# Kernel tuning notes

Hardware: AMD Instinct MI355X
Metric: run time of the kernel (lower is better)

The kernel has to match this reference:

```python
import jax, jax.numpy as jnp
import numpy as np

N, E, H, D_IN, D_OUT, DEPTH, G = 100000, 1600000, 128, 128, 10, 3, 256


def setup_inputs() -> dict:
    key = jax.random.key(0)
    ks = jax.random.split(key, 16)
    s = lambda k, shape: jax.random.normal(k, shape, dtype=jnp.float32) * 0.05
    inp = {
        "x": jax.random.normal(ks[0], (N, D_IN), dtype=jnp.float32),
        "edge_index": jax.random.randint(ks[1], (2, E), 0, N, dtype=jnp.int32),
        "control_edge_index": jax.random.randint(ks[2], (2, 1024), 0, N, dtype=jnp.int32),
        "batch": jnp.sort(jax.random.randint(ks[3], (N,), 0, G, dtype=jnp.int32)),
        # encoder MLP: input_dim -> hidden -> hidden
        "enc_w1": s(ks[4], (D_IN, H)), "enc_b1": jnp.zeros((H,), jnp.float32),
        "enc_w2": s(ks[5], (H, H)),    "enc_b2": jnp.zeros((H,), jnp.float32),
        # conv_depth GCN layers, hidden -> hidden
        "conv_w": s(ks[6], (DEPTH, H, H)), "conv_b": jnp.zeros((DEPTH, H), jnp.float32),
        # decoder MLP: hidden -> hidden -> output_dim
        "dec_w1": s(ks[7], (H, H)),     "dec_b1": jnp.zeros((H,), jnp.float32),
        "dec_w2": s(ks[8], (H, D_OUT)), "dec_b2": jnp.zeros((D_OUT,), jnp.float32),
    }
    return inp


def _gcn_forward(x, enc_w1, enc_b1, enc_w2, enc_b2, conv_w, conv_b,
                 dec_w1, dec_b1, dec_w2, dec_b2, edge_index, batch):
    # encoder MLP (Linear-ReLU-Dropout(eval)-Linear)
    h = jax.nn.relu(x @ enc_w1 + enc_b1) @ enc_w2 + enc_b2

    # GCN normalization with self-loops: D^{-1/2} (A + I) D^{-1/2}
    loops = jnp.arange(N, dtype=edge_index.dtype)
    src = jnp.concatenate([edge_index[0], loops])  # [E + N]
    dst = jnp.concatenate([edge_index[1], loops])
    deg = jax.ops.segment_sum(jnp.ones_like(src, dtype=h.dtype), dst, num_segments=N)
    inv_sqrt = jax.lax.rsqrt(deg)  # deg >= 1 thanks to self-loops
    coef = (inv_sqrt[src] * inv_sqrt[dst])[:, None]  # [E+N, 1]

    for l in range(DEPTH):
        hw = h @ conv_w[l] + conv_b[l]                      # [N, H]
        h = jax.ops.segment_sum(hw[src] * coef, dst, num_segments=N)
        if l < DEPTH - 1:  # linear=False -> nonlinearity between convs
            h = jax.nn.relu(h)

    # global_add_pool over graph ids
    pooled = jax.ops.segment_sum(h, batch, num_segments=G)   # [G, H]

    # decoder MLP
    return jax.nn.relu(pooled @ dec_w1 + dec_b1) @ dec_w2 + dec_b2  # [G, D_OUT]


def reference(x, edge_index, control_edge_index, batch, enc_w1, enc_b1, enc_w2,
              enc_b2, conv_w, conv_b, dec_w1, dec_b1, dec_w2, dec_b2):
    # control_edge_index corresponds to the (disabled) control mechanism; unused
    return _gcn_forward(x, enc_w1, enc_b1, enc_w2, enc_b2, conv_w, conv_b,
                        dec_w1, dec_b1, dec_w2, dec_b2, edge_index, batch)
```

## Files before the change

kernel.cpp:

```cpp
#include <hip/hip_runtime.h>
#include <hip/hip_bf16.h>
#include <cstdint>
#include <cstddef>

#define NN 100000
#define NE 1600000
#define HH 128
#define NG 256

#define NB 196
#define BSH 9
#define BMSK 511
#define CHUNK 16384
#define NBLK 98

typedef __bf16 bf16x8 __attribute__((ext_vector_type(8)));
typedef float floatx4 __attribute__((ext_vector_type(4)));

__device__ __forceinline__ uint32_t f2b(float f) {
  union { float f; uint32_t u; } v; v.f = f;
  uint32_t u = v.u;
  return (u + 0x7FFFu + ((u >> 16) & 1u)) >> 16;
}
__device__ __forceinline__ float b2f(uint32_t h) {
  union { uint32_t u; float f; } v; v.u = h << 16;
  return v.f;
}
__device__ __forceinline__ void addrow(float* a, uint4 v) {
  a[0] += b2f(v.x & 0xFFFFu); a[1] += b2f(v.x >> 16);
  a[2] += b2f(v.y & 0xFFFFu); a[3] += b2f(v.y >> 16);
  a[4] += b2f(v.z & 0xFFFFu); a[5] += b2f(v.z >> 16);
  a[6] += b2f(v.w & 0xFFFFu); a[7] += b2f(v.w >> 16);
}


__global__ __launch_bounds__(256) void k_cntA(const int* __restrict__ src,
                                              int* __restrict__ blkcnt) {
  __shared__ int h[NB];
  int t = threadIdx.x;
  if (t < NB) h[t] = 0;
  __syncthreads();
  int base = blockIdx.x * CHUNK, end = min(base + CHUNK, NE);
  for (int i = base + t; i < end; i += 256) atomicAdd(&h[src[i] >> BSH], 1);
  __syncthreads();
  if (t < NB) blkcnt[blockIdx.x * NB + t] = h[t];
}

__global__ __launch_bounds__(256) void k_cntB(const uint2* __restrict__ pairs,
                                              int* __restrict__ blkcnt) {
  __shared__ int h[NB];
  int t = threadIdx.x;
  if (t < NB) h[t] = 0;
  __syncthreads();
  int base = blockIdx.x * CHUNK, end = min(base + CHUNK, NE);
  for (int i = base + t; i < end; i += 256) atomicAdd(&h[pairs[i].y >> BSH], 1);
  __syncthreads();
  if (t < NB) blkcnt[blockIdx.x * NB + t] = h[t];
}

__global__ __launch_bounds__(64) void k_colscan(const int* __restrict__ blkcnt,
                                                int* __restrict__ poff,
                                                int* __restrict__ colsum) {
  int b = blockIdx.x, t = threadIdx.x;
  int carry = 0;
  for (int base = 0; base < NBLK; base += 64) {
    int r = base + t;
    int x = (r < NBLK) ? blkcnt[r * NB + b] : 0;
    int v = x;
    for (int d = 1; d < 64; d <<= 1) { int u = __shfl_up(v, d); if (t >= d) v += u; }
    if (r < NBLK) poff[r * NB + b] = carry + v - x;
    carry += __shfl(v, 63);
  }
  if (t == 0) colsum[b] = carry;
}

__global__ void k_gscan(const int* __restrict__ colsum, int* __restrict__ gbase,
                        int* __restrict__ off, int set_off) {
  __shared__ int s[256];
  int t = threadIdx.x;
  int x = (t < NB) ? colsum[t] : 0;
  s[t] = x; __syncthreads();
  for (int d = 1; d < 256; d <<= 1) {
    int v = (t >= d) ? s[t - d] : 0;
    __syncthreads();
    s[t] += v;
    __syncthreads();
  }
  if (t < NB) gbase[t] = s[t] - x;
  if (t == 0) { gbase[NB] = NE; if (set_off) off[NN] = NE; }
}

__global__ __launch_bounds__(256) void k_placeA(const int* __restrict__ src,
                                                const int* __restrict__ dst,
                                                const int* __restrict__ poff,
                                                const int* __restrict__ gbase,
                                                uint2* __restrict__ pairs) {
  __shared__ int cur[NB];
  int t = threadIdx.x;
  if (t < NB) cur[t] = poff[blockIdx.x * NB + t] + gbase[t];
  __syncthreads();
  int base = blockIdx.x * CHUNK, end = min(base + CHUNK, NE);
  for (int i = base + t; i < end; i += 256) {
    int s = src[i], d = dst[i];
    int p = atomicAdd(&cur[s >> BSH], 1);
    pairs[p] = make_uint2((unsigned)s, (unsigned)d);
  }
}

__global__ __launch_bounds__(256) void k_placeB(const uint2* __restrict__ pairs,
                                                const int* __restrict__ poff,
                                                const int* __restrict__ gbase,
                                                uint32_t* __restrict__ outb) {
  __shared__ int cur[NB];
  int t = threadIdx.x;
  if (t < NB) cur[t] = poff[blockIdx.x * NB + t] + gbase[t];
  __syncthreads();
  int base = blockIdx.x * CHUNK, end = min(base + CHUNK, NE);
  for (int i = base + t; i < end; i += 256) {
    uint2 v = pairs[i];
    int p = atomicAdd(&cur[v.y >> BSH], 1);
    outb[p] = v.x | ((v.y & (unsigned)BMSK) << 17);
  }
}

__global__ __launch_bounds__(256) void k_bucket_sort(
    const uint32_t* __restrict__ pairbuf, const int* __restrict__ gbase,
    const int* __restrict__ batch,
    int* __restrict__ off, float* __restrict__ inv, int* __restrict__ csrs,
    int* __restrict__ dhist2, int* __restrict__ gstart)
{
  __shared__ int cnt[512];
  __shared__ int loff[512];
  __shared__ int psum[256];
  int b = blockIdx.x;
  int tid = threadIdx.x;
  cnt[tid] = 0; cnt[tid + 256] = 0;
  __syncthreads();
  int s0 = gbase[b], s1 = gbase[b + 1];
  for (int i = s0 + tid; i < s1; i += 256)
    atomicAdd(&cnt[pairbuf[i] >> 17], 1);
  __syncthreads();
  int a0 = cnt[2 * tid], a1 = cnt[2 * tid + 1];
  int s = a0 + a1;
  psum[tid] = s;
  __syncthreads();
  for (int d = 1; d < 256; d <<= 1) {
    int v = (tid >= d) ? psum[tid - d] : 0;
    __syncthreads();
    psum[tid] += v;
    __syncthreads();
  }
  int excl = psum[tid] - s;
  loff[2 * tid] = excl;
  loff[2 * tid + 1] = excl + a0;
  __syncthreads();
  int* h64 = psum;
  if (tid < 64) h64[tid] = 0;
  __syncthreads();
#pragma unroll
  for (int k = 0; k < 2; ++k) {
    int i = tid + k * 256;
    int node = b * 512 + i;
    if (node < NN) {
      off[node] = s0 + loff[i];
      inv[node] = rsqrtf((float)cnt[i] + 1.0f);
      int d = cnt[i]; if (d > 63) d = 63;
      atomicAdd(&h64[d], 1);
    }
  }
  {
    int n0 = b * 512, n1 = min(n0 + 512, NN);
    for (int i = n0 + tid; i < n1; i += 256) {
      int bb = batch[i];
      if (i == 0) { for (int g = 0; g <= bb; ++g) gstart[g] = 0; }
      else { int aa = batch[i - 1]; for (int g = aa + 1; g <= bb; ++g) gstart[g] = i; }
      if (i == NN - 1) { for (int g = bb + 1; g <= NG; ++g) gstart[g] = NN; }
    }
  }
  __syncthreads();
  if (tid < 64) dhist2[b * 64 + tid] = h64[tid];
  cnt[tid] = loff[tid]; cnt[tid + 256] = loff[tid + 256];
  __syncthreads();
  for (int i = s0 + tid; i < s1; i += 256) {
    uint32_t v = pairbuf[i];
    int p = atomicAdd(&cnt[v >> 17], 1);
    csrs[s0 + p] = (int)(v & 0x1FFFFu);
  }
}

__global__ void k_dscan(const int* __restrict__ dhist2, int* __restrict__ dcur) {
  int t = threadIdx.x;
  int sum = 0;
  for (int r = 0; r < NB; ++r) sum += dhist2[r * 64 + (63 - t)];
  int v = sum;
  for (int d = 1; d < 64; d <<= 1) { int u = __shfl_up(v, d); if (t >= d) v += u; }
  dcur[63 - t] = v - sum;
}

__global__ __launch_bounds__(256) void k_dplace(const int* __restrict__ off,
                                                int* __restrict__ dcur,
                                                int* __restrict__ order) {
  __shared__ int h[64], base[64];
  int t = threadIdx.x;
  if (t < 64) h[t] = 0;
  __syncthreads();
  int i = blockIdx.x * 256 + t;
  int d = 0, ld = 0;
  if (i < NN) { d = off[i + 1] - off[i]; if (d > 63) d = 63; ld = atomicAdd(&h[d], 1); }
  __syncthreads();
  if (t < 64) base[t] = h[t] ? atomicAdd(&dcur[t], h[t]) : 0;
  __syncthreads();
  if (i < NN) order[base[d] + ld] = i;
}

__global__ __launch_bounds__(256) void k_gemm(
    const uint16_t* __restrict__ A16, const float* __restrict__ A32,
    const float* __restrict__ W, const float* __restrict__ bias,
    const float* __restrict__ scale,
    uint16_t* __restrict__ Out, int M, int do_relu)
{
  __shared__ uint16_t Wt[128][136];
  const int tid = threadIdx.x;

  for (int it = 0; it < 16; ++it) {
    int idx = tid + it * 256;
    int n = idx & 127;
    int k0 = (idx >> 7) * 4;
    uint2 wv;
    wv.x = f2b(W[(k0 + 0) * 128 + n]) | (f2b(W[(k0 + 1) * 128 + n]) << 16);
    wv.y = f2b(W[(k0 + 2) * 128 + n]) | (f2b(W[(k0 + 3) * 128 + n]) << 16);
    *(uint2*)&Wt[n][k0] = wv;
  }
  __syncthreads();

  const int lane = tid & 63;
  const int wave = tid >> 6;
  const int lrow = lane & 15;
  const int quad = lane >> 4;
  const int lk = quad * 8;
  const int row0 = blockIdx.x * 128 + wave * 32;

  floatx4 acc[2][8];
#pragma unroll
  for (int t = 0; t < 2; ++t)
#pragma unroll
    for (int n = 0; n < 8; ++n)
      acc[t][n] = (floatx4){0.f, 0.f, 0.f, 0.f};

#pragma unroll
  for (int ks = 0; ks < 4; ++ks) {
    bf16x8 a[2];
#pragma unroll
    for (int t = 0; t < 2; ++t) {
      int r = row0 + t * 16 + lrow;
      uint4 tmp = {0u, 0u, 0u, 0u};
      if (r < M) {
        if (A32) {
          float4 f0 = *(const float4*)(A32 + (size_t)r * HH + ks * 32 + lk);
          float4 f1 = *(const float4*)(A32 + (size_t)r * HH + ks * 32 + lk + 4);
          tmp.x = f2b(f0.x) | (f2b(f0.y) << 16);
          tmp.y = f2b(f0.z) | (f2b(f0.w) << 16);
          tmp.z = f2b(f1.x) | (f2b(f1.y) << 16);
          tmp.w = f2b(f1.z) | (f2b(f1.w) << 16);
        } else {
          tmp = *(const uint4*)(A16 + (size_t)r * HH + ks * 32 + lk);
        }
      }
      a[t] = __builtin_bit_cast(bf16x8, tmp);
    }
#pragma unroll
    for (int n = 0; n < 8; ++n) {
      bf16x8 b = __builtin_bit_cast(bf16x8, *(const uint4*)&Wt[n * 16 + lrow][ks * 32 + lk]);
      acc[0][n] = __builtin_amdgcn_mfma_f32_16x16x32_bf16(b, a[0], acc[0][n], 0, 0, 0);
      acc[1][n] = __builtin_amdgcn_mfma_f32_16x16x32_bf16(b, a[1], acc[1][n], 0, 0, 0);
    }
  }

  float4 b4[8];
#pragma unroll
  for (int n = 0; n < 8; ++n) b4[n] = *(const float4*)(bias + n * 16 + quad * 4);

#pragma unroll
  for (int t = 0; t < 2; ++t) {
    int row = row0 + t * 16 + lrow;
    if (row < M) {
      float sc = scale ? scale[row] : 1.0f;
      uint16_t* orow = Out + (size_t)row * HH;
#pragma unroll
      for (int n = 0; n < 8; ++n) {
        float v0 = acc[t][n][0] + b4[n].x;
        float v1 = acc[t][n][1] + b4[n].y;
        float v2 = acc[t][n][2] + b4[n].z;
        float v3 = acc[t][n][3] + b4[n].w;
        if (do_relu) {
          v0 = fmaxf(v0, 0.f); v1 = fmaxf(v1, 0.f);
          v2 = fmaxf(v2, 0.f); v3 = fmaxf(v3, 0.f);
        }
        v0 *= sc; v1 *= sc; v2 *= sc; v3 *= sc;
        uint2 o;
        o.x = f2b(v0) | (f2b(v1) << 16);
        o.y = f2b(v2) | (f2b(v3) << 16);
        *(uint2*)(orow + n * 16 + quad * 4) = o;
      }
    }
  }
}

__global__ __launch_bounds__(256) void k_agg(
    const uint16_t* __restrict__ hw2, const int* __restrict__ off,
    const int* __restrict__ csrs, const float* __restrict__ inv,
    const int* __restrict__ order,
    uint16_t* __restrict__ hout, int do_relu)
{
  int slot = blockIdx.x * 16 + (threadIdx.x >> 4);
  if (slot >= NN) return;
  int node = order[slot];
  int c = (threadIdx.x & 15) * 8;

  uint4 sv = *(const uint4*)(hw2 + (size_t)node * HH + c);
  float a[8] = {0.f, 0.f, 0.f, 0.f, 0.f, 0.f, 0.f, 0.f};
  addrow(a, sv);

  int e0 = off[node], e1 = off[node + 1];
  int e = e0;
  for (; e + 4 <= e1; e += 4) {
    int s0 = csrs[e + 0], s1 = csrs[e + 1], s2 = csrs[e + 2], s3 = csrs[e + 3];
    uint4 v0 = *(const uint4*)(hw2 + (size_t)s0 * HH + c);
    uint4 v1 = *(const uint4*)(hw2 + (size_t)s1 * HH + c);
    uint4 v2 = *(const uint4*)(hw2 + (size_t)s2 * HH + c);
    uint4 v3 = *(const uint4*)(hw2 + (size_t)s3 * HH + c);
    addrow(a, v0); addrow(a, v1); addrow(a, v2); addrow(a, v3);
  }
  for (; e < e1; ++e) {
    int s = csrs[e];
    uint4 v = *(const uint4*)(hw2 + (size_t)s * HH + c);
    addrow(a, v);
  }
  float invd = inv[node];
#pragma unroll
  for (int j = 0; j < 8; ++j) {
    a[j] *= invd;
    if (do_relu) a[j] = fmaxf(a[j], 0.f);
  }
  uint4 o;
  o.x = f2b(a[0]) | (f2b(a[1]) << 16);
  o.y = f2b(a[2]) | (f2b(a[3]) << 16);
  o.z = f2b(a[4]) | (f2b(a[5]) << 16);
  o.w = f2b(a[6]) | (f2b(a[7]) << 16);
  *(uint4*)(hout + (size_t)node * HH + c) = o;
}

__global__ __launch_bounds__(256) void k_pooldec(
    const uint16_t* __restrict__ h, const int* __restrict__ gstart,
    const float* __restrict__ w1, const float* __restrict__ b1,
    const float* __restrict__ w2, const float* __restrict__ b2,
    float* __restrict__ out)
{
  __shared__ float red[16][132];
  __shared__ float p[128], tmpv[128];
  int g = blockIdx.x;
  int tid = threadIdx.x;
  int slot = tid >> 4;
  int c = (tid & 15) * 8;

  int r0 = gstart[g], r1 = gstart[g + 1];
  float a[8] = {0.f, 0.f, 0.f, 0.f, 0.f, 0.f, 0.f, 0.f};
  for (int r = r0 + slot; r < r1; r += 16) {
    uint4 v = *(const uint4*)(h + (size_t)r * HH + c);
    a[0] += b2f(v.x & 0xFFFFu); a[1] += b2f(v.x >> 16);
    a[2] += b2f(v.y & 0xFFFFu); a[3] += b2f(v.y >> 16);
    a[4] += b2f(v.z & 0xFFFFu); a[5] += b2f(v.z >> 16);
    a[6] += b2f(v.w & 0xFFFFu); a[7] += b2f(v.w >> 16);
  }
  *(float4*)&red[slot][c]     = make_float4(a[0], a[1], a[2], a[3]);
  *(float4*)&red[slot][c + 4] = make_float4(a[4], a[5], a[6], a[7]);
  __syncthreads();
  if (tid < 128) {
    float s = 0.f;
#pragma unroll
    for (int k = 0; k < 16; ++k) s += red[k][tid];
    p[tid] = s;
  }
  __syncthreads();
  if (tid < 128) {
    float acc1 = b1[tid];
    for (int k = 0; k < 128; ++k) acc1 += p[k] * w1[k * 128 + tid];
    tmpv[tid] = fmaxf(acc1, 0.f);
  }
  __syncthreads();
  if (tid < 10) {
    float o = b2[tid];
    for (int k = 0; k < 128; ++k) o += tmpv[k] * w2[k * 10 + tid];
    out[g * 10 + tid] = o;
  }
}

extern "C" void kernel_launch(void* const* d_in, const int* in_sizes, int n_in,
                              void* d_out, int out_size, void* d_ws, size_t ws_size,
                              hipStream_t stream) {
  const float* x       = (const float*)d_in[0];
  const int*   eidx    = (const int*)d_in[1];
  const int*   src     = eidx;
  const int*   dst     = eidx + NE;
  const int*   batch   = (const int*)d_in[3];
  const float* enc_w1  = (const float*)d_in[4];
  const float* enc_b1  = (const float*)d_in[5];
  const float* enc_w2  = (const float*)d_in[6];
  const float* enc_b2  = (const float*)d_in[7];
  const float* conv_w  = (const float*)d_in[8];
  const float* conv_b  = (const float*)d_in[9];
  const float* dec_w1  = (const float*)d_in[10];
  const float* dec_b1  = (const float*)d_in[11];
  const float* dec_w2  = (const float*)d_in[12];
  const float* dec_b2  = (const float*)d_in[13];
  float* out = (float*)d_out;

  char* ws = (char*)d_ws;
  size_t o = 0;
  auto alloc = [&](size_t bytes) -> char* {
    char* p = ws + o;
    o += (bytes + 255) & ~(size_t)255;
    return p;
  };
  int*      off     = (int*)alloc((size_t)(NN + 1) * 4);
  int*      csrs    = (int*)alloc((size_t)NE * 4);
  float*    inv     = (float*)alloc((size_t)NN * 4);
  int*      blkcntA = (int*)alloc((size_t)NBLK * NB * 4);
  int*      poffA   = (int*)alloc((size_t)NBLK * NB * 4);
  int*      blkcntB = (int*)alloc((size_t)NBLK * NB * 4);
  int*      poffB   = (int*)alloc((size_t)NBLK * NB * 4);
  int*      colsumA = (int*)alloc((size_t)NB * 4);
  int*      colsumB = (int*)alloc((size_t)NB * 4);
  int*      gbaseA  = (int*)alloc((size_t)(NB + 1) * 4);
  int*      gbaseB  = (int*)alloc((size_t)(NB + 1) * 4);
  int*      dhist2  = (int*)alloc((size_t)NB * 64 * 4);
  int*      dcur    = (int*)alloc(64 * 4);
  int*      order   = (int*)alloc((size_t)NN * 4);
  int*      gstart  = (int*)alloc((size_t)(NG + 1) * 4);
  uint16_t* buf0    = (uint16_t*)alloc((size_t)NN * HH * 2);
  uint16_t* buf1    = (uint16_t*)alloc((size_t)NN * HH * 2);
  uint2*    pairsA  = (uint2*)buf1;
  uint32_t* pairB   = (uint32_t*)((char*)buf1 + (size_t)NE * 8);

  k_cntA<<<dim3(NBLK), dim3(256), 0, stream>>>(src, blkcntA);
  k_colscan<<<dim3(NB), dim3(64), 0, stream>>>(blkcntA, poffA, colsumA);
  k_gscan<<<dim3(1), dim3(256), 0, stream>>>(colsumA, gbaseA, off, 0);
  k_placeA<<<dim3(NBLK), dim3(256), 0, stream>>>(src, dst, poffA, gbaseA, pairsA);
  k_cntB<<<dim3(NBLK), dim3(256), 0, stream>>>(pairsA, blkcntB);
  k_colscan<<<dim3(NB), dim3(64), 0, stream>>>(blkcntB, poffB, colsumB);
  k_gscan<<<dim3(1), dim3(256), 0, stream>>>(colsumB, gbaseB, off, 1);
  k_placeB<<<dim3(NBLK), dim3(256), 0, stream>>>(pairsA, poffB, gbaseB, pairB);
  k_bucket_sort<<<dim3(NB), dim3(256), 0, stream>>>(pairB, gbaseB, batch, off, inv, csrs,
                                                    dhist2, gstart);

  const int NBK = (NN + 255) / 256;
  k_dscan<<<dim3(1), dim3(64), 0, stream>>>(dhist2, dcur);
  k_dplace<<<dim3(NBK), dim3(256), 0, stream>>>(off, dcur, order);

  const int GB = (NN + 127) / 128;
  k_gemm<<<dim3(GB), dim3(256), 0, stream>>>(nullptr, x, enc_w1, enc_b1, nullptr, buf1, NN, 1);
  k_gemm<<<dim3(GB), dim3(256), 0, stream>>>(buf1, nullptr, enc_w2, enc_b2, nullptr, buf0, NN, 0);

  const int AB = (NN + 15) / 16;
  k_gemm<<<dim3(GB), dim3(256), 0, stream>>>(buf0, nullptr, conv_w + 0 * 16384, conv_b + 0,   inv, buf1, NN, 0);
  k_agg <<<dim3(AB), dim3(256), 0, stream>>>(buf1, off, csrs, inv, order, buf0, 1);
  k_gemm<<<dim3(GB), dim3(256), 0, stream>>>(buf0, nullptr, conv_w + 1 * 16384, conv_b + 128, inv, buf1, NN, 0);
  k_agg <<<dim3(AB), dim3(256), 0, stream>>>(buf1, off, csrs, inv, order, buf0, 1);
  k_gemm<<<dim3(GB), dim3(256), 0, stream>>>(buf0, nullptr, conv_w + 2 * 16384, conv_b + 256, inv, buf1, NN, 0);
  k_agg <<<dim3(AB), dim3(256), 0, stream>>>(buf1, off, csrs, inv, order, buf0, 0);

  k_pooldec<<<dim3(NG), dim3(256), 0, stream>>>(buf0, gstart, dec_w1, dec_b1, dec_w2, dec_b2, out);
}
```

Baseline: 527.3 us.

## Fuse encoder second linear with first GCN weight GEMM; merge scan kernels

Adds a dual-GEMM kernel that computes the encoder's second linear layer into a shared-memory bf16 tile, then immediately multiplies it by the first conv weight. This removes one full N×H bf16 write and read to global memory and one kernel launch. The two-kernel column scan plus global scan is also replaced by one single-block scan kernel, which saves launches but serializes the per-bucket column sums. The fused kernel doubles shared-memory use, which may reduce occupancy. It also adds an extra intermediate bf16 rounding, which the old path already had.

```diff
diff --git a/kernel.cpp b/kernel.cpp
--- a/kernel.cpp
+++ b/kernel.cpp
@@ -33,6 +33,19 @@
   a[6] += b2f(v.w & 0xFFFFu); a[7] += b2f(v.w >> 16);
 }
 
+__device__ __forceinline__ void stage_w(uint16_t (*Wt)[136], const float* __restrict__ W,
+                                        int tid) {
+  for (int it = 0; it < 16; ++it) {
+    int idx = tid + it * 256;
+    int n = idx & 127;
+    int k0 = (idx >> 7) * 4;
+    uint2 wv;
+    wv.x = f2b(W[(k0 + 0) * 128 + n]) | (f2b(W[(k0 + 1) * 128 + n]) << 16);
+    wv.y = f2b(W[(k0 + 2) * 128 + n]) | (f2b(W[(k0 + 3) * 128 + n]) << 16);
+    *(uint2*)&Wt[n][k0] = wv;
+  }
+}
+
 
 __global__ __launch_bounds__(256) void k_cntA(const int* __restrict__ src,
                                               int* __restrict__ blkcnt) {
@@ -58,35 +71,26 @@
   if (t < NB) blkcnt[blockIdx.x * NB + t] = h[t];
 }
 
-__global__ __launch_bounds__(64) void k_colscan(const int* __restrict__ blkcnt,
-                                                int* __restrict__ poff,
-                                                int* __restrict__ colsum) {
-  int b = blockIdx.x, t = threadIdx.x;
-  int carry = 0;
-  for (int base = 0; base < NBLK; base += 64) {
-    int r = base + t;
-    int x = (r < NBLK) ? blkcnt[r * NB + b] : 0;
-    int v = x;
-    for (int d = 1; d < 64; d <<= 1) { int u = __shfl_up(v, d); if (t >= d) v += u; }
-    if (r < NBLK) poff[r * NB + b] = carry + v - x;
-    carry += __shfl(v, 63);
-  }
-  if (t == 0) colsum[b] = carry;
-}
-
-__global__ void k_gscan(const int* __restrict__ colsum, int* __restrict__ gbase,
-                        int* __restrict__ off, int set_off) {
+__global__ void k_scan(const int* __restrict__ blkcnt, int* __restrict__ poff,
+                       int* __restrict__ gbase, int* __restrict__ off, int set_off) {
   __shared__ int s[256];
   int t = threadIdx.x;
-  int x = (t < NB) ? colsum[t] : 0;
-  s[t] = x; __syncthreads();
+  int tot = 0;
+  if (t < NB) {
+    for (int r = 0; r < NBLK; ++r) {
+      poff[r * NB + t] = tot;
+      tot += blkcnt[r * NB + t];
+    }
+  }
+  s[t] = (t < NB) ? tot : 0;
+  __syncthreads();
   for (int d = 1; d < 256; d <<= 1) {
     int v = (t >= d) ? s[t - d] : 0;
     __syncthreads();
     s[t] += v;
     __syncthreads();
   }
-  if (t < NB) gbase[t] = s[t] - x;
+  if (t < NB) gbase[t] = s[t] - tot;
   if (t == 0) { gbase[NB] = NE; if (set_off) off[NN] = NE; }
 }
 
@@ -221,16 +225,7 @@
 {
   __shared__ uint16_t Wt[128][136];
   const int tid = threadIdx.x;
-
-  for (int it = 0; it < 16; ++it) {
-    int idx = tid + it * 256;
-    int n = idx & 127;
-    int k0 = (idx >> 7) * 4;
-    uint2 wv;
-    wv.x = f2b(W[(k0 + 0) * 128 + n]) | (f2b(W[(k0 + 1) * 128 + n]) << 16);
-    wv.y = f2b(W[(k0 + 2) * 128 + n]) | (f2b(W[(k0 + 3) * 128 + n]) << 16);
-    *(uint2*)&Wt[n][k0] = wv;
-  }
+  stage_w(Wt, W, tid);
   __syncthreads();
 
   const int lane = tid & 63;
@@ -301,6 +296,118 @@
         o.x = f2b(v0) | (f2b(v1) << 16);
         o.y = f2b(v2) | (f2b(v3) << 16);
         *(uint2*)(orow + n * 16 + quad * 4) = o;
+      }
+    }
+  }
+}
+
+__global__ __launch_bounds__(256) void k_gemm_dual(
+    const uint16_t* __restrict__ A16,
+    const float* __restrict__ Wa, const float* __restrict__ ba,
+    const float* __restrict__ Wb, const float* __restrict__ bb,
+    const float* __restrict__ scale,
+    uint16_t* __restrict__ Out, int M)
+{
+  __shared__ uint16_t Wt[128][136];
+  __shared__ uint16_t tile[128][136];
+  const int tid = threadIdx.x;
+  stage_w(Wt, Wa, tid);
+  __syncthreads();
+
+  const int lane = tid & 63;
+  const int wave = tid >> 6;
+  const int lrow = lane & 15;
+  const int quad = lane >> 4;
+  const int lk = quad * 8;
+  const int row0 = blockIdx.x * 128 + wave * 32;
+  const int trow0 = wave * 32;
+
+  floatx4 acc[2][8];
+#pragma unroll
+  for (int t = 0; t < 2; ++t)
+#pragma unroll
+    for (int n = 0; n < 8; ++n)
+      acc[t][n] = (floatx4){0.f, 0.f, 0.f, 0.f};
+
+#pragma unroll
+  for (int ks = 0; ks < 4; ++ks) {
+    bf16x8 a[2];
+#pragma unroll
+    for (int t = 0; t < 2; ++t) {
+      int r = row0 + t * 16 + lrow;
+      uint4 tmp = {0u, 0u, 0u, 0u};
+      if (r < M) tmp = *(const uint4*)(A16 + (size_t)r * HH + ks * 32 + lk);
+      a[t] = __builtin_bit_cast(bf16x8, tmp);
+    }
+#pragma unroll
+    for (int n = 0; n < 8; ++n) {
+      bf16x8 b = __builtin_bit_cast(bf16x8, *(const uint4*)&Wt[n * 16 + lrow][ks * 32 + lk]);
+      acc[0][n] = __builtin_amdgcn_mfma_f32_16x16x32_bf16(b, a[0], acc[0][n], 0, 0, 0);
+      acc[1][n] = __builtin_amdgcn_mfma_f32_16x16x32_bf16(b, a[1], acc[1][n], 0, 0, 0);
+    }
+  }
+
+  {
+    float4 b4[8];
+#pragma unroll
+    for (int n = 0; n < 8; ++n) b4[n] = *(const float4*)(ba + n * 16 + quad * 4);
+#pragma unroll
+    for (int t = 0; t < 2; ++t) {
+      int trow = trow0 + t * 16 + lrow;
+#pragma unroll
+      for (int n = 0; n < 8; ++n) {
+        uint2 o;
+        o.x = f2b(acc[t][n][0] + b4[n].x) | (f2b(acc[t][n][1] + b4[n].y) << 16);
+        o.y = f2b(acc[t][n][2] + b4[n].z) | (f2b(acc[t][n][3] + b4[n].w) << 16);
+        *(uint2*)&tile[trow][n * 16 + quad * 4] = o;
+      }
+    }
+  }
+  __syncthreads();
+  stage_w(Wt, Wb, tid);
+#pragma unroll
+  for (int t = 0; t < 2; ++t)
+#pragma unroll
+    for (int n = 0; n < 8; ++n)
+      acc[t][n] = (floatx4){0.f, 0.f, 0.f, 0.f};
+  __syncthreads();
+
+#pragma unroll
+  for (int ks = 0; ks < 4; ++ks) {
+    bf16x8 a[2];
+#pragma unroll
+    for (int t = 0; t < 2; ++t)
+      a[t] = __builtin_bit_cast(bf16x8,
+               *(const uint4*)&tile[trow0 + t * 16 + lrow][ks * 32 + lk]);
+#pragma unroll
+    for (int n = 0; n < 8; ++n) {
+      bf16x8 b = __builtin_bit_cast(bf16x8, *(const uint4*)&Wt[n * 16 + lrow][ks * 32 + lk]);
+      acc[0][n] = __builtin_amdgcn_mfma_f32_16x16x32_bf16(b, a[0], acc[0][n], 0, 0, 0);
+      acc[1][n] = __builtin_amdgcn_mfma_f32_16x16x32_bf16(b, a[1], acc[1][n], 0, 0, 0);
+    }
+  }
+
+  {
+    float4 b4[8];
+#pragma unroll
+    for (int n = 0; n < 8; ++n) b4[n] = *(const float4*)(bb + n * 16 + quad * 4);
+#pragma unroll
+    for (int t = 0; t < 2; ++t) {
+      int row = row0 + t * 16 + lrow;
+      if (row < M) {
+        float sc = scale ? scale[row] : 1.0f;
+        uint16_t* orow = Out + (size_t)row * HH;
+#pragma unroll
+        for (int n = 0; n < 8; ++n) {
+          float v0 = (acc[t][n][0] + b4[n].x) * sc;
+          float v1 = (acc[t][n][1] + b4[n].y) * sc;
+          float v2 = (acc[t][n][2] + b4[n].z) * sc;
+          float v3 = (acc[t][n][3] + b4[n].w) * sc;
+          uint2 o;
+          o.x = f2b(v0) | (f2b(v1) << 16);
+          o.y = f2b(v2) | (f2b(v3) << 16);
+          *(uint2*)(orow + n * 16 + quad * 4) = o;
+        }
       }
     }
   }
@@ -429,8 +536,6 @@
   int*      poffA   = (int*)alloc((size_t)NBLK * NB * 4);
   int*      blkcntB = (int*)alloc((size_t)NBLK * NB * 4);
   int*      poffB   = (int*)alloc((size_t)NBLK * NB * 4);
-  int*      colsumA = (int*)alloc((size_t)NB * 4);
-  int*      colsumB = (int*)alloc((size_t)NB * 4);
   int*      gbaseA  = (int*)alloc((size_t)(NB + 1) * 4);
   int*      gbaseB  = (int*)alloc((size_t)(NB + 1) * 4);
   int*      dhist2  = (int*)alloc((size_t)NB * 64 * 4);
@@ -443,12 +548,10 @@
   uint32_t* pairB   = (uint32_t*)((char*)buf1 + (size_t)NE * 8);
 
   k_cntA<<<dim3(NBLK), dim3(256), 0, stream>>>(src, blkcntA);
-  k_colscan<<<dim3(NB), dim3(64), 0, stream>>>(blkcntA, poffA, colsumA);
-  k_gscan<<<dim3(1), dim3(256), 0, stream>>>(colsumA, gbaseA, off, 0);
+  k_scan<<<dim3(1), dim3(256), 0, stream>>>(blkcntA, poffA, gbaseA, off, 0);
   k_placeA<<<dim3(NBLK), dim3(256), 0, stream>>>(src, dst, poffA, gbaseA, pairsA);
   k_cntB<<<dim3(NBLK), dim3(256), 0, stream>>>(pairsA, blkcntB);
-  k_colscan<<<dim3(NB), dim3(64), 0, stream>>>(blkcntB, poffB, colsumB);
-  k_gscan<<<dim3(1), dim3(256), 0, stream>>>(colsumB, gbaseB, off, 1);
+  k_scan<<<dim3(1), dim3(256), 0, stream>>>(blkcntB, poffB, gbaseB, off, 1);
   k_placeB<<<dim3(NBLK), dim3(256), 0, stream>>>(pairsA, poffB, gbaseB, pairB);
   k_bucket_sort<<<dim3(NB), dim3(256), 0, stream>>>(pairB, gbaseB, batch, off, inv, csrs,
                                                     dhist2, gstart);
@@ -459,15 +562,16 @@
 
   const int GB = (NN + 127) / 128;
   k_gemm<<<dim3(GB), dim3(256), 0, stream>>>(nullptr, x, enc_w1, enc_b1, nullptr, buf1, NN, 1);
-  k_gemm<<<dim3(GB), dim3(256), 0, stream>>>(buf1, nullptr, enc_w2, enc_b2, nullptr, buf0, NN, 0);
+  k_gemm_dual<<<dim3(GB), dim3(256), 0, stream>>>(buf1, enc_w2, enc_b2,
+                                                  conv_w + 0 * 16384, conv_b + 0,
+                                                  inv, buf0, NN);
 
   const int AB = (NN + 15) / 16;
-  k_gemm<<<dim3(GB), dim3(256), 0, stream>>>(buf0, nullptr, conv_w + 0 * 16384, conv_b + 0,   inv, buf1, NN, 0);
-  k_agg <<<dim3(AB), dim3(256), 0, stream>>>(buf1, off, csrs, inv, order, buf0, 1);
-  k_gemm<<<dim3(GB), dim3(256), 0, stream>>>(buf0, nullptr, conv_w + 1 * 16384, conv_b + 128, inv, buf1, NN, 0);
-  k_agg <<<dim3(AB), dim3(256), 0, stream>>>(buf1, off, csrs, inv, order, buf0, 1);
-  k_gemm<<<dim3(GB), dim3(256), 0, stream>>>(buf0, nullptr, conv_w + 2 * 16384, conv_b + 256, inv, buf1, NN, 0);
-  k_agg <<<dim3(AB), dim3(256), 0, stream>>>(buf1, off, csrs, inv, order, buf0, 0);
-
-  k_pooldec<<<dim3(NG), dim3(256), 0, stream>>>(buf0, gstart, dec_w1, dec_b1, dec_w2, dec_b2, out);
-}
+  k_agg <<<dim3(AB), dim3(256), 0, stream>>>(buf0, off, csrs, inv, order, buf1, 1);
+  k_gemm<<<dim3(GB), dim3(256), 0, stream>>>(buf1, nullptr, conv_w + 1 * 16384, conv_b + 128, inv, buf0, NN, 0);
+  k_agg <<<dim3(AB), dim3(256), 0, stream>>>(buf0, off, csrs, inv, order, buf1, 1);
+  k_gemm<<<dim3(GB), dim3(256), 0, stream>>>(buf1, nullptr, conv_w + 2 * 16384, conv_b + 256, inv, buf0, NN, 0);
+  k_agg <<<dim3(AB), dim3(256), 0, stream>>>(buf0, off, csrs, inv, order, buf1, 0);
+
+  k_pooldec<<<dim3(NG), dim3(256), 0, stream>>>(buf1, gstart, dec_w1, dec_b1, dec_w2, dec_b2, out);
+}
```

Result: no change. 518.7 us (-1.6%).
